# Optimization experiments

Hardware: AMD Instinct MI355X
Metric: run time of the kernel (lower is better)

Reference implementation:

```python
import jax, jax.numpy as jnp
import numpy as np
from jax import lax

B, J, I = 32, 48, 48          # batch, target len, source len
W = 2                          # target_window_size
CTX = 2 * W + 1                # 5
E, H = 128, 256                # embedding_size, hidden_units
VT, VS = 32000, 32000          # target / source vocab
S = 2 * J                      # HMM states (word + null)


def setup_inputs() -> dict:
    key = jax.random.key(0)
    ks = jax.random.split(key, 12)
    inp = {
        "target_embedding": jax.random.normal(ks[0], (VT, E), jnp.float32) * 0.02,
        "W_bridge": jax.random.normal(ks[1], (E * CTX, E), jnp.float32) * 0.02,
        "W_hidden": jax.random.normal(ks[2], (E, H), jnp.float32) * 0.02,
        "b_hidden": jnp.zeros((H,), jnp.float32),
        "W_vocab": jax.random.normal(ks[3], (H, VS), jnp.float32) * 0.02,
        "b_vocab": jnp.zeros((VS,), jnp.float32),
        "transition": jax.random.uniform(ks[4], (B, S, S), jnp.float32, 0.01, 1.0),
        "initial_transition": jax.random.uniform(ks[5], (B, S), jnp.float32, 0.01, 1.0),
        "targets_ctx": jax.random.randint(ks[6], (B, J * CTX), 0, VT, jnp.int32),
        "targets_ctx_null": jax.random.randint(ks[7], (B, J * CTX), 0, VT, jnp.int32),
        "sources": jax.random.randint(ks[8], (B, I), 0, VS, jnp.int32),
    }
    return inp


def _emission(emb, Wb, Wh, bh, Wv, bv, ctx_ids, sources):
    # embedding lookup + context reshape: [B, J*CTX, E] -> [B, J, CTX*E]
    x = emb[ctx_ids].reshape(ctx_ids.shape[0], -1, CTX * E)
    h = jnp.tanh(jnp.einsum('bjc,ce,eh->bjh', x, Wb, Wh) + bh)  # bridge+hidden
    probs = jax.nn.softmax(h @ Wv + bv, axis=-1)                # [B, J, VS]
    # per-example gather of source token columns -> [B, J, I]
    return jax.vmap(lambda p, s: p[:, s])(probs, sources)


def _forward_backward(pi, A, em):
    # pi [B,S], A [B,S,S], em [B,S,I]; scaled HMM forward-backward
    e = jnp.moveaxis(em, 2, 0)  # [I, B, S]
    a0 = pi * e[0]
    c0 = a0.sum(-1, keepdims=True)
    a0 = a0 / c0

    def fstep(a, ei):
        an = jnp.einsum('bs,bst->bt', a, A) * ei
        c = an.sum(-1, keepdims=True)
        an = an / c
        return an, (an, c)

    _, (alphas, cs) = lax.scan(fstep, a0, e[1:])
    alphas = jnp.concatenate([a0[None], alphas], 0)          # [I,B,S]
    cs = jnp.concatenate([c0[None], cs], 0)                  # [I,B,1]

    def bstep(b, inp):
        ei, ci = inp
        bn = jnp.einsum('bst,bt->bs', A, ei * b) / ci
        return bn, bn

    bI = jnp.ones_like(a0)
    _, betas_rev = lax.scan(bstep, bI, (e[1:][::-1], cs[1:][::-1]))
    betas = jnp.concatenate([betas_rev[::-1], bI[None]], 0)  # [I,B,S]

    gamma = alphas * betas                                   # state posteriors
    loglik = jnp.log(cs[..., 0]).sum(0)                      # [B]
    return jnp.moveaxis(gamma, 0, 2), loglik


def reference(target_embedding, W_bridge, W_hidden, b_hidden, W_vocab, b_vocab,
              transition, initial_transition, targets_ctx, targets_ctx_null, sources):
    em_word = _emission(target_embedding, W_bridge, W_hidden, b_hidden,
                        W_vocab, b_vocab, targets_ctx, sources)       # [B,J,I]
    em_null = _emission(target_embedding, W_bridge, W_hidden, b_hidden,
                        W_vocab, b_vocab, targets_ctx_null, sources)  # [B,J,I]
    emission = jnp.concatenate([em_word, em_null], axis=1)            # [B,2J,I]
    gamma, loglik = _forward_backward(initial_transition, transition, emission)
    return gamma, -loglik
```

## Files before the change

### kernel.cpp

```cpp
#include <hip/hip_runtime.h>
#include <hip/hip_bf16.h>

#define NB 32
#define NJ 48
#define NI 48
#define NCTX 5
#define NE 128
#define NH 256
#define NVS 32000
#define NS 96
#define NR 3072

typedef __attribute__((ext_vector_type(8))) short bf16x8;
typedef __attribute__((ext_vector_type(4))) float f32x4;

__device__ __forceinline__ unsigned short f2b(float f) {
  __hip_bfloat16 h = __float2bfloat16(f);
  return *reinterpret_cast<unsigned short*>(&h);
}
__device__ __forceinline__ float wave_sum(float v) {
  v += __shfl_xor(v, 1);
  v += __shfl_xor(v, 2);
  v += __shfl_xor(v, 4);
  v += __shfl_xor(v, 8);
  v += __shfl_xor(v, 16);
  v += __shfl_xor(v, 32);
  return v;
}
__device__ __forceinline__ void gload_lds16(const void* g, void* l) {
  __builtin_amdgcn_global_load_lds(
      (const __attribute__((address_space(1))) void*)g,
      (__attribute__((address_space(3))) void*)l, 16, 0, 0);
}


__global__ __launch_bounds__(256) void k_transpose(const float* __restrict__ Wv,
                                                   unsigned char* __restrict__ Wv8) {
  __shared__ float tile[64][65];
  int t = threadIdx.x;
  int v0 = blockIdx.x * 64, k0 = blockIdx.y * 64;
  {
    int kr = t >> 4, vq = t & 15;
#pragma unroll
    for (int it = 0; it < 4; ++it) {
      float4 v = *(const float4*)&Wv[(k0 + kr + 16 * it) * NVS + v0 + vq * 4];
      tile[kr + 16 * it][vq * 4 + 0] = v.x;
      tile[kr + 16 * it][vq * 4 + 1] = v.y;
      tile[kr + 16 * it][vq * 4 + 2] = v.z;
      tile[kr + 16 * it][vq * 4 + 3] = v.w;
    }
  }
  __syncthreads();
  {
    int vl = t >> 2, kq = t & 3;
    unsigned int q8[4];
#pragma unroll
    for (int d = 0; d < 4; ++d) {
      float f0 = tile[kq * 16 + d * 4 + 0][vl] * 64.0f;
      float f1 = tile[kq * 16 + d * 4 + 1][vl] * 64.0f;
      float f2 = tile[kq * 16 + d * 4 + 2][vl] * 64.0f;
      float f3 = tile[kq * 16 + d * 4 + 3][vl] * 64.0f;
      int w = __builtin_amdgcn_cvt_pk_fp8_f32(f0, f1, 0, false);
      w = __builtin_amdgcn_cvt_pk_fp8_f32(f2, f3, w, true);
      q8[d] = (unsigned int)w;
    }
    int kqp = kq ^ ((vl >> 2) & 3);
    unsigned int q8s[4];
    if ((vl >> 1) & 1) {
      q8s[0] = q8[2]; q8s[1] = q8[3]; q8s[2] = q8[0]; q8s[3] = q8[1];
    } else {
      q8s[0] = q8[0]; q8s[1] = q8[1]; q8s[2] = q8[2]; q8s[3] = q8[3];
    }
    *(uint4*)&Wv8[(v0 + vl) * 256 + k0 + kqp * 16] = *(uint4*)q8s;
  }
}

__global__ __launch_bounds__(256) void k_t2b(const float* __restrict__ src,
                                             unsigned short* __restrict__ dst,
                                             int R, int C) {
  __shared__ float tile[64][65];
  int t = threadIdx.x;
  int r0 = blockIdx.x * 64, c0 = blockIdx.y * 64;
  {
    int rr = t >> 4, cq = t & 15;
#pragma unroll
    for (int it = 0; it < 4; ++it) {
      float4 v = *(const float4*)&src[(r0 + rr + 16 * it) * C + c0 + cq * 4];
      tile[rr + 16 * it][cq * 4 + 0] = v.x;
      tile[rr + 16 * it][cq * 4 + 1] = v.y;
      tile[rr + 16 * it][cq * 4 + 2] = v.z;
      tile[rr + 16 * it][cq * 4 + 3] = v.w;
    }
  }
  __syncthreads();
  {
    int cc = t >> 2, rq = t & 3;
    unsigned short pk[16];
#pragma unroll
    for (int q = 0; q < 16; ++q) pk[q] = f2b(tile[rq * 16 + q][cc]);
    *(uint4*)&dst[(c0 + cc) * R + r0 + rq * 16] = *(uint4*)&pk[0];
    *(uint4*)&dst[(c0 + cc) * R + r0 + rq * 16 + 8] = *(uint4*)&pk[8];
  }
}

__global__ __launch_bounds__(256) void k_xb(const float* __restrict__ emb,
                                            const unsigned short* __restrict__ Wbt,
                                            const int* __restrict__ tc, const int* __restrict__ tcn,
                                            unsigned short* __restrict__ xb) {
  __shared__ unsigned short Ax[32 * 72];
  __shared__ unsigned short Bw[128 * 72];
  __shared__ unsigned short xout[32 * 136];
  int t = threadIdx.x;
  int r0 = blockIdx.x * 32;
  int wave = t >> 6, lane = t & 63;
  int wm = wave >> 1, wn = wave & 1;
  int lg = lane >> 4, lr = lane & 15;
  int arow = t >> 3, aseg = t & 7;
  int r = r0 + arow;
  int half = r / 1536, rem = r % 1536, bb = rem / 48, jj = rem % 48;
  const int* ids = half ? tcn : tc;
  int brow = t >> 1, bseg = t & 1;

  f32x4 acc[4];
#pragma unroll
  for (int n = 0; n < 4; ++n) acc[n] = (f32x4){0.f, 0.f, 0.f, 0.f};

  for (int step = 0; step < 10; ++step) {
    int k0 = step * 64;
    int p = step >> 1;
    int e0 = (step & 1) * 64;
    {
      int id = ids[bb * 240 + jj * 5 + p];
      const float4* er = (const float4*)&emb[id * 128 + e0 + aseg * 8];
      float4 v0 = er[0], v1 = er[1];
      unsigned short pk[8];
      pk[0] = f2b(v0.x); pk[1] = f2b(v0.y); pk[2] = f2b(v0.z); pk[3] = f2b(v0.w);
      pk[4] = f2b(v1.x); pk[5] = f2b(v1.y); pk[6] = f2b(v1.z); pk[7] = f2b(v1.w);
      *(uint4*)&Ax[arow * 72 + aseg * 8] = *(uint4*)&pk[0];
    }
    {
      const uint4* wp = (const uint4*)&Wbt[brow * 640 + k0 + bseg * 32];
      uint4* dp = (uint4*)&Bw[brow * 72 + bseg * 32];
      uint4 w0 = wp[0], w1 = wp[1], w2 = wp[2], w3 = wp[3];
      dp[0] = w0; dp[1] = w1; dp[2] = w2; dp[3] = w3;
    }
    __syncthreads();
#pragma unroll
    for (int kk = 0; kk < 2; ++kk) {
      bf16x8 a = *(const bf16x8*)&Ax[(wm * 16 + lr) * 72 + kk * 32 + lg * 8];
#pragma unroll
      for (int n = 0; n < 4; ++n) {
        bf16x8 b = *(const bf16x8*)&Bw[(wn * 64 + n * 16 + lr) * 72 + kk * 32 + lg * 8];
        acc[n] = __builtin_amdgcn_mfma_f32_16x16x32_bf16(a, b, acc[n], 0, 0, 0);
      }
    }
    __syncthreads();
  }
#pragma unroll
  for (int n = 0; n < 4; ++n)
#pragma unroll
    for (int g = 0; g < 4; ++g)
      xout[(wm * 16 + lg * 4 + g) * 136 + wn * 64 + n * 16 + lr] = f2b(acc[n][g]);
  __syncthreads();
  {
    int orow = t >> 3, os = t & 7;
    *(uint4*)&xb[(r0 + orow) * 128 + os * 16] = *(uint4*)&xout[orow * 136 + os * 16];
    *(uint4*)&xb[(r0 + orow) * 128 + os * 16 + 8] = *(uint4*)&xout[orow * 136 + os * 16 + 8];
  }
}

__global__ __launch_bounds__(256) void k_h(const unsigned short* __restrict__ xb,
                                           const unsigned short* __restrict__ Wht,
                                           const float* __restrict__ bh,
                                           unsigned char* __restrict__ hb8) {
  __shared__ char smem[69632];
  unsigned short* Asm = (unsigned short*)smem;
  unsigned short* Bsm = (unsigned short*)(smem + 34816);
  unsigned char* o8 = (unsigned char*)smem;
  int t = threadIdx.x;
  int r0 = blockIdx.x * 128, n0 = blockIdx.y * 128;
  int wave = t >> 6, lane = t & 63;
  int wm = wave >> 1, wn = wave & 1;
  int lg = lane >> 4, lr = lane & 15;
  {
    int row = t >> 1, seg = t & 1;
#pragma unroll
    for (int i = 0; i < 8; ++i) {
      *(uint4*)&Asm[row * 136 + seg * 64 + i * 8] = *(const uint4*)&xb[(r0 + row) * 128 + seg * 64 + i * 8];
      *(uint4*)&Bsm[row * 136 + seg * 64 + i * 8] = *(const uint4*)&Wht[(n0 + row) * 128 + seg * 64 + i * 8];
    }
  }
  __syncthreads();
  f32x4 acc[4][4];
#pragma unroll
  for (int m = 0; m < 4; ++m)
#pragma unroll
    for (int n = 0; n < 4; ++n) acc[m][n] = (f32x4){0.f, 0.f, 0.f, 0.f};
#pragma unroll
  for (int kk = 0; kk < 4; ++kk) {
    bf16x8 a[4], b[4];
#pragma unroll
    for (int m = 0; m < 4; ++m)
      a[m] = *(const bf16x8*)&Asm[(wm * 64 + m * 16 + lr) * 136 + kk * 32 + lg * 8];
#pragma unroll
    for (int n = 0; n < 4; ++n)
      b[n] = *(const bf16x8*)&Bsm[(wn * 64 + n * 16 + lr) * 136 + kk * 32 + lg * 8];
#pragma unroll
    for (int m = 0; m < 4; ++m)
#pragma unroll
      for (int n = 0; n < 4; ++n)
        acc[m][n] = __builtin_amdgcn_mfma_f32_16x16x32_bf16(a[m], b[n], acc[m][n], 0, 0, 0);
  }
  __syncthreads();
#pragma unroll
  for (int n = 0; n < 4; ++n) {
    int cl = wn * 64 + n * 16 + lr;
    float bvv = bh[n0 + cl];
#pragma unroll
    for (int m = 0; m < 4; ++m) {
#pragma unroll
      for (int g = 0; g < 4; ++g) {
        int rl = wm * 64 + m * 16 + lg * 4 + g;
        float hv = tanhf(acc[m][n][g] + bvv);
        int p8 = __builtin_amdgcn_cvt_pk_fp8_f32(hv * 256.0f, 0.0f, 0, false);
        o8[rl * 144 + cl] = (unsigned char)(p8 & 0xFF);
      }
    }
  }
  __syncthreads();
  {
    int row = t >> 1, seg = t & 1;
    int sig = (row >> 1) & 7;
    int swp = row & 1;
#pragma unroll
    for (int i = 0; i < 4; ++i) {
      int p_loc = seg * 4 + i;
      int w_loc = p_loc ^ sig;
      unsigned long long q[2];
      q[0] = *(const unsigned long long*)&o8[row * 144 + w_loc * 16 + swp * 8];
      q[1] = *(const unsigned long long*)&o8[row * 144 + w_loc * 16 + (swp ^ 1) * 8];
      *(uint4*)&hb8[(r0 + row) * 256 + n0 + p_loc * 16] = *(uint4*)q;
    }
  }
}

__global__ __launch_bounds__(256) void k_denom(const unsigned char* __restrict__ hb8,
                                               const unsigned char* __restrict__ Wv8,
                                               const float* __restrict__ bv,
                                               float* __restrict__ dpart) {
  __shared__ __align__(16) unsigned char Asm[32768];
  int t = threadIdx.x;
  int bid = blockIdx.x;
  int xcd = bid & 7;
  int pos = bid >> 3;
  int tile = xcd * 375 + pos;
  int vtp = tile / 24, rt = tile % 24;
  int r0 = rt * 128;
  int wave = t >> 6, lane = t & 63;
  int wm = wave >> 1, wn = wave & 1;
  int lg = lane >> 4, lr = lane & 15;

#pragma unroll
  for (int c = 0; c < 8; ++c) {
    int inst = wave * 8 + c;
    gload_lds16(&hb8[(r0 + inst * 4 + (lane >> 4)) * 256 + (lane & 15) * 16], &Asm[inst * 1024]);
  }
  __syncthreads();

  long long a_reg[4][8];
#pragma unroll
  for (int m = 0; m < 4; ++m) {
    int rowb = (wm * 64 + m * 16 + lr) * 256;
#pragma unroll
    for (int s = 0; s < 8; ++s)
      a_reg[m][s] = *(const long long*)&Asm[rowb + (((s * 4 + lg) ^ lr) << 3)];
  }

  const float SC = 6.103515625e-05f;
  int sg = (lr >> 1) & 7;

#pragma unroll
  for (int vt = 0; vt < 2; ++vt) {
    const unsigned char* Bp = Wv8 + ((size_t)((vtp * 2 + vt) * 128 + wn * 64 + lr)) * 256;
    f32x4 acc[4][4];
#pragma unroll
    for (int m = 0; m < 4; ++m)
#pragma unroll
      for (int n = 0; n < 4; ++n) acc[m][n] = (f32x4){0.f, 0.f, 0.f, 0.f};

#pragma unroll
    for (int ks = 0; ks < 4; ++ks) {
#pragma unroll
      for (int kk = 0; kk < 2; ++kk) {
        int so = ks * 64 + ((((kk << 2) + lg) ^ sg) << 3);
        long long b[4];
#pragma unroll
        for (int n = 0; n < 4; ++n)
          b[n] = *(const long long*)(Bp + n * 4096 + so);
        __builtin_amdgcn_s_setprio(1);
#pragma unroll
        for (int m = 0; m < 4; ++m)
#pragma unroll
          for (int n = 0; n < 4; ++n)
            acc[m][n] = __builtin_amdgcn_mfma_f32_16x16x32_fp8_fp8(a_reg[m][ks * 2 + kk], b[n],
                                                                   acc[m][n], 0, 0, 0);
        __builtin_amdgcn_s_setprio(0);
      }
    }
    int v0 = (vtp * 2 + vt) * 128;
    float rs[4][4];
#pragma unroll
    for (int m = 0; m < 4; ++m)
#pragma unroll
      for (int g = 0; g < 4; ++g) rs[m][g] = 0.f;
#pragma unroll
    for (int m = 0; m < 4; ++m) {
#pragma unroll
      for (int n = 0; n < 4; ++n) {
        float bvv = bv[v0 + wn * 64 + n * 16 + lr];
#pragma unroll
        for (int g = 0; g < 4; ++g) rs[m][g] += __expf(acc[m][n][g] * SC + bvv);
      }
    }
#pragma unroll
    for (int m = 0; m < 4; ++m)
#pragma unroll
      for (int g = 0; g < 4; ++g) {
        float v = rs[m][g];
        v += __shfl_xor(v, 1);
        v += __shfl_xor(v, 2);
        v += __shfl_xor(v, 4);
        v += __shfl_xor(v, 8);
        rs[m][g] = v;
      }
    if (lr == 0) {
      int d = (vtp * 2 + vt) * 2 + wn;
#pragma unroll
      for (int m = 0; m < 4; ++m)
#pragma unroll
        for (int g = 0; g < 4; ++g)
          dpart[d * NR + r0 + wm * 64 + m * 16 + lg * 4 + g] = rs[m][g];
    }
  }
}

__global__ void k_reduce(const float* __restrict__ dpart, float* __restrict__ dsum) {
  int r = blockIdx.x * 256 + threadIdx.x;
  float s = 0.f;
  for (int vt = 0; vt < 500; ++vt) s += dpart[vt * NR + r];
  dsum[r] = s;
}

__global__ __launch_bounds__(64) void k_emis(const unsigned char* __restrict__ hb8,
                                             const unsigned char* __restrict__ Wv8,
                                             const float* __restrict__ bv,
                                             const float* __restrict__ dsum,
                                             const int* __restrict__ src,
                                             float* __restrict__ em) {
  __shared__ unsigned char A8[48 * 256];
  __shared__ unsigned char B8[48 * 256];
  __shared__ int s_src[48];
  int t = threadIdx.x;
  int bh = blockIdx.x;
  int b = bh & 31, half = bh >> 5;
  int row4 = t >> 4, seg = t & 15;
  int rbase = half * 1536 + b * 48;
  if (t < 48) s_src[t] = src[b * 48 + t];
#pragma unroll
  for (int c = 0; c < 12; ++c) {
    int row = c * 4 + row4;
    gload_lds16(&hb8[(rbase + row) * 256 + seg * 16], &A8[c * 1024]);
    int sv = src[b * 48 + row];
    gload_lds16(&Wv8[sv * 256 + seg * 16], &B8[c * 1024]);
  }
  __syncthreads();
  int lg = t >> 4, lr = t & 15;
  int svr[3];
#pragma unroll
  for (int m = 0; m < 3; ++m) svr[m] = s_src[m * 16 + lr];
  f32x4 acc[3][3];
#pragma unroll
  for (int m = 0; m < 3; ++m)
#pragma unroll
    for (int n = 0; n < 3; ++n) acc[m][n] = (f32x4){0.f, 0.f, 0.f, 0.f};
#pragma unroll
  for (int kk = 0; kk < 8; ++kk) {
    int sa = kk * 4 + lg;
    long long a[3], bb[3];
#pragma unroll
    for (int m = 0; m < 3; ++m) {
      int rr = m * 16 + lr;
      a[m] = *(const long long*)&A8[rr * 256 + ((sa ^ lr) << 3)];
      bb[m] = *(const long long*)&B8[rr * 256 + ((sa >> 3) << 6) +
                                     (((sa & 7) ^ ((svr[m] >> 1) & 7)) << 3)];
    }
#pragma unroll
    for (int m = 0; m < 3; ++m)
#pragma unroll
      for (int n = 0; n < 3; ++n)
        acc[m][n] = __builtin_amdgcn_mfma_f32_16x16x32_fp8_fp8(a[m], bb[n], acc[m][n], 0, 0, 0);
  }
  const float SC = 6.103515625e-05f;
#pragma unroll
  for (int n = 0; n < 3; ++n) {
    int i = n * 16 + lr;
    float bvv = bv[svr[n]];
#pragma unroll
    for (int m = 0; m < 3; ++m) {
#pragma unroll
      for (int g = 0; g < 4; ++g) {
        int j = m * 16 + lg * 4 + g;
        float val = __expf(acc[m][n][g] * SC + bvv) / dsum[rbase + j];
        em[b * 4608 + (half * 48 + j) * 48 + i] = val;
      }
    }
  }
}

__global__ __launch_bounds__(192) void k_fb(const float* __restrict__ Atr, const float* __restrict__ pi,
                                            const float* __restrict__ em, float* __restrict__ alph,
                                            float* __restrict__ betas, float* __restrict__ out1) {
  __shared__ float A_st[96 * 97];
  __shared__ float em_lds[48 * 97];
  __shared__ __align__(16) float vec_lds[96];
  __shared__ float red[3];
  int t = threadIdx.x;
  int bid = blockIdx.x;
  int b = bid & 31;
  int role = bid >> 5;
  int col = t >> 1, half = t & 1;
  int base = b * 4608;

  for (int idx = t; idx < 96 * 96; idx += 192) {
    int s = idx / 96, tt = idx % 96;
    A_st[s * 97 + tt] = Atr[b * 9216 + idx];
  }
  for (int idx = t; idx < 96 * 48; idx += 192) {
    int s = idx / 48, i = idx % 48;
    em_lds[i * 97 + s] = em[base + idx];
  }
  __syncthreads();

  float Areg[48];
  if (role == 0) {
#pragma unroll
    for (int ss = 0; ss < 48; ++ss) Areg[ss] = A_st[(half * 48 + ss) * 97 + col];

    float llsum;
    {
      float v = pi[b * 96 + col] * em_lds[0 * 97 + col];
      float ws = half ? 0.f : v;
      ws = wave_sum(ws);
      if ((t & 63) == 0) red[t >> 6] = ws;
      __syncthreads();
      float c = red[0] + red[1] + red[2];
      float a = v / c;
      if (!half) {
        vec_lds[col] = a;
        alph[base + col] = a;
      }
      llsum = logf(c);
      __syncthreads();
    }
    for (int i = 1; i < 48; ++i) {
      float p = 0.f;
      const float4* ap = (const float4*)&vec_lds[half * 48];
#pragma unroll
      for (int q = 0; q < 12; ++q) {
        float4 av = ap[q];
        p += av.x * Areg[4 * q] + av.y * Areg[4 * q + 1] + av.z * Areg[4 * q + 2] + av.w * Areg[4 * q + 3];
      }
      p += __shfl_xor(p, 1);
      float an = p * em_lds[i * 97 + col];
      float ws = half ? 0.f : an;
      ws = wave_sum(ws);
      if ((t & 63) == 0) red[t >> 6] = ws;
      __syncthreads();
      float c = red[0] + red[1] + red[2];
      float a = an / c;
      if (!half) {
        vec_lds[col] = a;
        alph[base + i * 96 + col] = a;
      }
      llsum += logf(c);
      __syncthreads();
    }
    if (t == 0) out1[b] = -llsum;
  } else {
#pragma unroll
    for (int tt = 0; tt < 48; ++tt) Areg[tt] = A_st[col * 97 + half * 48 + tt];

    if (!half) {
      betas[base + 47 * 96 + col] = 1.0f;
      vec_lds[col] = em_lds[47 * 97 + col];
    }
    __syncthreads();
    for (int i = 46; i >= 0; --i) {
      float p = 0.f;
      const float4* ep = (const float4*)&vec_lds[half * 48];
#pragma unroll
      for (int q = 0; q < 12; ++q) {
        float4 ev = ep[q];
        p += ev.x * Areg[4 * q] + ev.y * Areg[4 * q + 1] + ev.z * Areg[4 * q + 2] + ev.w * Areg[4 * q + 3];
      }
      p += __shfl_xor(p, 1);
      float ws = half ? 0.f : p;
      ws = wave_sum(ws);
      if ((t & 63) == 0) red[t >> 6] = ws;
      __syncthreads();
      float c = red[0] + red[1] + red[2];
      float bt = p / c;
      if (!half) {
        betas[base + i * 96 + col] = bt;
        vec_lds[col] = em_lds[i * 97 + col] * bt;
      }
      __syncthreads();
    }
  }
}

__global__ __launch_bounds__(128) void k_gamma(const float* __restrict__ alph,
                                               const float* __restrict__ betas,
                                               float* __restrict__ out0) {
  __shared__ float red[2];
  int b = blockIdx.x, i = blockIdx.y;
  int t = threadIdx.x;
  float g = 0.f;
  if (t < 96) g = alph[b * 4608 + i * 96 + t] * betas[b * 4608 + i * 96 + t];
  float ws = wave_sum(g);
  if ((t & 63) == 0) red[t >> 6] = ws;
  __syncthreads();
  float c = red[0] + red[1];
  if (t < 96) out0[b * 4608 + t * 48 + i] = g / c;
}

extern "C" void kernel_launch(void* const* d_in, const int* in_sizes, int n_in,
                              void* d_out, int out_size, void* d_ws, size_t ws_size,
                              hipStream_t stream) {
  const float* emb = (const float*)d_in[0];
  const float* Wb  = (const float*)d_in[1];
  const float* Wh  = (const float*)d_in[2];
  const float* bh  = (const float*)d_in[3];
  const float* Wv  = (const float*)d_in[4];
  const float* bv  = (const float*)d_in[5];
  const float* Atr = (const float*)d_in[6];
  const float* pi  = (const float*)d_in[7];
  const int* tc    = (const int*)d_in[8];
  const int* tcn   = (const int*)d_in[9];
  const int* src   = (const int*)d_in[10];

  float* out0 = (float*)d_out;
  float* out1 = out0 + NB * NS * NI;

  char* ws = (char*)d_ws;
  unsigned char* wv8 = (unsigned char*)(ws);
  unsigned char* hb8 = (unsigned char*)(ws + 8192000);
  float* dpart       = (float*)(ws + 8978432);
  float* betas       = (float*)(ws + 8978432);
  float* dsum        = (float*)(ws + 15122432);
  float* em          = (float*)(ws + 15134720);
  float* alph        = (float*)(ws + 15724544);
  unsigned short* wbt = (unsigned short*)(ws + 16314368);
  unsigned short* wht = (unsigned short*)(ws + 16478208);
  unsigned short* xb  = (unsigned short*)(ws + 16543744);

  k_transpose<<<dim3(500, 4), 256, 0, stream>>>(Wv, wv8);
  k_t2b<<<dim3(10, 2), 256, 0, stream>>>(Wb, wbt, 640, 128);
  k_t2b<<<dim3(2, 4), 256, 0, stream>>>(Wh, wht, 128, 256);
  k_xb<<<96, 256, 0, stream>>>(emb, wbt, tc, tcn, xb);
  k_h<<<dim3(24, 2), 256, 0, stream>>>(xb, wht, bh, hb8);
  k_denom<<<3000, 256, 0, stream>>>(hb8, wv8, bv, dpart);
  k_reduce<<<12, 256, 0, stream>>>(dpart, dsum);
  k_emis<<<64, 64, 0, stream>>>(hb8, wv8, bv, dsum, src, em);
  k_fb<<<64, 192, 0, stream>>>(Atr, pi, em, alph, betas, out1);
  k_gamma<<<dim3(32, 48), 128, 0, stream>>>(alph, betas, out0);
}
```

Measured before the change: 168.8 us.

## Merge weight prep kernels, stage Wv8 through double-buffered LDS in denom, widen reduce

```diff
diff --git a/kernel.cpp b/kernel.cpp
--- a/kernel.cpp
+++ b/kernel.cpp
@@ -34,53 +34,11 @@
 }
 
 
-__global__ __launch_bounds__(256) void k_transpose(const float* __restrict__ Wv,
-                                                   unsigned char* __restrict__ Wv8) {
-  __shared__ float tile[64][65];
-  int t = threadIdx.x;
-  int v0 = blockIdx.x * 64, k0 = blockIdx.y * 64;
-  {
-    int kr = t >> 4, vq = t & 15;
-#pragma unroll
-    for (int it = 0; it < 4; ++it) {
-      float4 v = *(const float4*)&Wv[(k0 + kr + 16 * it) * NVS + v0 + vq * 4];
-      tile[kr + 16 * it][vq * 4 + 0] = v.x;
-      tile[kr + 16 * it][vq * 4 + 1] = v.y;
-      tile[kr + 16 * it][vq * 4 + 2] = v.z;
-      tile[kr + 16 * it][vq * 4 + 3] = v.w;
-    }
-  }
-  __syncthreads();
-  {
-    int vl = t >> 2, kq = t & 3;
-    unsigned int q8[4];
-#pragma unroll
-    for (int d = 0; d < 4; ++d) {
-      float f0 = tile[kq * 16 + d * 4 + 0][vl] * 64.0f;
-      float f1 = tile[kq * 16 + d * 4 + 1][vl] * 64.0f;
-      float f2 = tile[kq * 16 + d * 4 + 2][vl] * 64.0f;
-      float f3 = tile[kq * 16 + d * 4 + 3][vl] * 64.0f;
-      int w = __builtin_amdgcn_cvt_pk_fp8_f32(f0, f1, 0, false);
-      w = __builtin_amdgcn_cvt_pk_fp8_f32(f2, f3, w, true);
-      q8[d] = (unsigned int)w;
-    }
-    int kqp = kq ^ ((vl >> 2) & 3);
-    unsigned int q8s[4];
-    if ((vl >> 1) & 1) {
-      q8s[0] = q8[2]; q8s[1] = q8[3]; q8s[2] = q8[0]; q8s[3] = q8[1];
-    } else {
-      q8s[0] = q8[0]; q8s[1] = q8[1]; q8s[2] = q8[2]; q8s[3] = q8[3];
-    }
-    *(uint4*)&Wv8[(v0 + vl) * 256 + k0 + kqp * 16] = *(uint4*)q8s;
-  }
-}
-
-__global__ __launch_bounds__(256) void k_t2b(const float* __restrict__ src,
-                                             unsigned short* __restrict__ dst,
-                                             int R, int C) {
-  __shared__ float tile[64][65];
-  int t = threadIdx.x;
-  int r0 = blockIdx.x * 64, c0 = blockIdx.y * 64;
+__device__ __forceinline__ void t2b_body(const float* __restrict__ src,
+                                         unsigned short* __restrict__ dst,
+                                         int R, int C, int bx, int by, int t,
+                                         float (*tile)[65]) {
+  int r0 = bx * 64, c0 = by * 64;
   {
     int rr = t >> 4, cq = t & 15;
 #pragma unroll
@@ -100,6 +58,60 @@
     for (int q = 0; q < 16; ++q) pk[q] = f2b(tile[rq * 16 + q][cc]);
     *(uint4*)&dst[(c0 + cc) * R + r0 + rq * 16] = *(uint4*)&pk[0];
     *(uint4*)&dst[(c0 + cc) * R + r0 + rq * 16 + 8] = *(uint4*)&pk[8];
+  }
+}
+
+__global__ __launch_bounds__(256) void k_prep(const float* __restrict__ Wv,
+                                              unsigned char* __restrict__ Wv8,
+                                              const float* __restrict__ Wb,
+                                              unsigned short* __restrict__ wbt,
+                                              const float* __restrict__ Wh,
+                                              unsigned short* __restrict__ wht) {
+  __shared__ float tile[64][65];
+  int t = threadIdx.x;
+  int blk = blockIdx.x;
+  if (blk < 2000) {
+    int v0 = (blk % 500) * 64, k0 = (blk / 500) * 64;
+    {
+      int kr = t >> 4, vq = t & 15;
+#pragma unroll
+      for (int it = 0; it < 4; ++it) {
+        float4 v = *(const float4*)&Wv[(k0 + kr + 16 * it) * NVS + v0 + vq * 4];
+        tile[kr + 16 * it][vq * 4 + 0] = v.x;
+        tile[kr + 16 * it][vq * 4 + 1] = v.y;
+        tile[kr + 16 * it][vq * 4 + 2] = v.z;
+        tile[kr + 16 * it][vq * 4 + 3] = v.w;
+      }
+    }
+    __syncthreads();
+    {
+      int vl = t >> 2, kq = t & 3;
+      unsigned int q8[4];
+#pragma unroll
+      for (int d = 0; d < 4; ++d) {
+        float f0 = tile[kq * 16 + d * 4 + 0][vl] * 64.0f;
+        float f1 = tile[kq * 16 + d * 4 + 1][vl] * 64.0f;
+        float f2 = tile[kq * 16 + d * 4 + 2][vl] * 64.0f;
+        float f3 = tile[kq * 16 + d * 4 + 3][vl] * 64.0f;
+        int w = __builtin_amdgcn_cvt_pk_fp8_f32(f0, f1, 0, false);
+        w = __builtin_amdgcn_cvt_pk_fp8_f32(f2, f3, w, true);
+        q8[d] = (unsigned int)w;
+      }
+      int kqp = kq ^ ((vl >> 2) & 3);
+      unsigned int q8s[4];
+      if ((vl >> 1) & 1) {
+        q8s[0] = q8[2]; q8s[1] = q8[3]; q8s[2] = q8[0]; q8s[3] = q8[1];
+      } else {
+        q8s[0] = q8[0]; q8s[1] = q8[1]; q8s[2] = q8[2]; q8s[3] = q8[3];
+      }
+      *(uint4*)&Wv8[(v0 + vl) * 256 + k0 + kqp * 16] = *(uint4*)q8s;
+    }
+  } else if (blk < 2020) {
+    int b = blk - 2000;
+    t2b_body(Wb, wbt, 640, 128, b % 10, b / 10, t, tile);
+  } else {
+    int b = blk - 2020;
+    t2b_body(Wh, wht, 128, 256, b % 2, b / 2, t, tile);
   }
 }
 
@@ -248,107 +260,137 @@
                                                const unsigned char* __restrict__ Wv8,
                                                const float* __restrict__ bv,
                                                float* __restrict__ dpart) {
-  __shared__ __align__(16) unsigned char Asm[32768];
+  __shared__ __align__(16) unsigned char smem[16384];
   int t = threadIdx.x;
   int bid = blockIdx.x;
   int xcd = bid & 7;
   int pos = bid >> 3;
-  int tile = xcd * 375 + pos;
-  int vtp = tile / 24, rt = tile % 24;
+  int tl = xcd * 375 + pos;
+  int vtp = tl / 24, rt = tl % 24;
   int r0 = rt * 128;
   int wave = t >> 6, lane = t & 63;
   int wm = wave >> 1, wn = wave & 1;
   int lg = lane >> 4, lr = lane & 15;
 
 #pragma unroll
-  for (int c = 0; c < 8; ++c) {
-    int inst = wave * 8 + c;
-    gload_lds16(&hb8[(r0 + inst * 4 + (lane >> 4)) * 256 + (lane & 15) * 16], &Asm[inst * 1024]);
-  }
-  __syncthreads();
+  for (int c = 0; c < 2; ++c) {
+    int i = wave * 2 + c;
+    gload_lds16(&Wv8[((size_t)(vtp * 256 + i * 16 + (lane >> 2))) * 256 + (lane & 3) * 16],
+                smem + i * 1024);
+  }
 
   long long a_reg[4][8];
 #pragma unroll
   for (int m = 0; m < 4; ++m) {
-    int rowb = (wm * 64 + m * 16 + lr) * 256;
-#pragma unroll
-    for (int s = 0; s < 8; ++s)
-      a_reg[m][s] = *(const long long*)&Asm[rowb + (((s * 4 + lg) ^ lr) << 3)];
+#pragma unroll
+    for (int c = 0; c < 2; ++c) {
+      int inst = wave * 2 + c;
+      int slot = inst * 4 + (lane >> 4);
+      int row = (slot & 15) + m * 16 + ((slot >> 4) << 6);
+      gload_lds16(&hb8[(size_t)(r0 + row) * 256 + (lane & 15) * 16],
+                  smem + 8192 + inst * 1024);
+    }
+    __syncthreads();
+    {
+      int q = lr + 16 * wm;
+#pragma unroll
+      for (int s = 0; s < 8; ++s)
+        a_reg[m][s] = *(const long long*)&smem[8192 + q * 256 + (((s * 4 + lg) ^ lr) << 3)];
+    }
+    __syncthreads();
   }
 
   const float SC = 6.103515625e-05f;
-  int sg = (lr >> 1) & 7;
-
-#pragma unroll
-  for (int vt = 0; vt < 2; ++vt) {
-    const unsigned char* Bp = Wv8 + ((size_t)((vtp * 2 + vt) * 128 + wn * 64 + lr)) * 256;
-    f32x4 acc[4][4];
-#pragma unroll
-    for (int m = 0; m < 4; ++m)
-#pragma unroll
-      for (int n = 0; n < 4; ++n) acc[m][n] = (f32x4){0.f, 0.f, 0.f, 0.f};
-
-#pragma unroll
-    for (int ks = 0; ks < 4; ++ks) {
-#pragma unroll
-      for (int kk = 0; kk < 2; ++kk) {
-        int so = ks * 64 + ((((kk << 2) + lg) ^ sg) << 3);
-        long long b[4];
+  f32x4 acc[4][4];
+#pragma unroll
+  for (int m = 0; m < 4; ++m)
+#pragma unroll
+    for (int n = 0; n < 4; ++n) acc[m][n] = (f32x4){0.f, 0.f, 0.f, 0.f};
+
+#pragma unroll
+  for (int s = 0; s < 8; ++s) {
+    if (s < 7) {
+      int ns = s + 1;
+      int nvt = ns >> 2, nks = ns & 3;
+#pragma unroll
+      for (int c = 0; c < 2; ++c) {
+        int i = wave * 2 + c;
+        gload_lds16(&Wv8[((size_t)((vtp * 2 + nvt) * 128 + i * 16 + (lane >> 2))) * 256 +
+                         nks * 64 + (lane & 3) * 16],
+                    smem + ((ns & 1) << 13) + i * 1024);
+      }
+    }
+    int ks = s & 3;
+    const unsigned char* bp = smem + ((s & 1) << 13);
+#pragma unroll
+    for (int kk = 0; kk < 2; ++kk) {
+      long long b[4];
+#pragma unroll
+      for (int n = 0; n < 4; ++n) {
+        int rr = wn * 64 + n * 16 + lr;
+        b[n] = *(const long long*)&bp[rr * 64 + ((((kk << 2) + lg) ^ ((lr >> 1) & 7)) << 3)];
+      }
+      __builtin_amdgcn_s_setprio(1);
+#pragma unroll
+      for (int m = 0; m < 4; ++m)
 #pragma unroll
         for (int n = 0; n < 4; ++n)
-          b[n] = *(const long long*)(Bp + n * 4096 + so);
-        __builtin_amdgcn_s_setprio(1);
+          acc[m][n] = __builtin_amdgcn_mfma_f32_16x16x32_fp8_fp8(a_reg[m][ks * 2 + kk], b[n],
+                                                                 acc[m][n], 0, 0, 0);
+      __builtin_amdgcn_s_setprio(0);
+    }
+    if (ks == 3) {
+      int vt = s >> 2;
+      int v0 = (vtp * 2 + vt) * 128;
+      float rs[4][4];
+#pragma unroll
+      for (int m = 0; m < 4; ++m)
+#pragma unroll
+        for (int g = 0; g < 4; ++g) rs[m][g] = 0.f;
+#pragma unroll
+      for (int m = 0; m < 4; ++m) {
+#pragma unroll
+        for (int n = 0; n < 4; ++n) {
+          float bvv = bv[v0 + wn * 64 + n * 16 + lr];
+#pragma unroll
+          for (int g = 0; g < 4; ++g) rs[m][g] += __expf(acc[m][n][g] * SC + bvv);
+          acc[m][n] = (f32x4){0.f, 0.f, 0.f, 0.f};
+        }
+      }
+#pragma unroll
+      for (int m = 0; m < 4; ++m)
+#pragma unroll
+        for (int g = 0; g < 4; ++g) {
+          float v = rs[m][g];
+          v += __shfl_xor(v, 1);
+          v += __shfl_xor(v, 2);
+          v += __shfl_xor(v, 4);
+          v += __shfl_xor(v, 8);
+          rs[m][g] = v;
+        }
+      if (lr == 0) {
+        int d = (vtp * 2 + vt) * 2 + wn;
 #pragma unroll
         for (int m = 0; m < 4; ++m)
 #pragma unroll
-          for (int n = 0; n < 4; ++n)
-            acc[m][n] = __builtin_amdgcn_mfma_f32_16x16x32_fp8_fp8(a_reg[m][ks * 2 + kk], b[n],
-                                                                   acc[m][n], 0, 0, 0);
-        __builtin_amdgcn_s_setprio(0);
-      }
-    }
-    int v0 = (vtp * 2 + vt) * 128;
-    float rs[4][4];
-#pragma unroll
-    for (int m = 0; m < 4; ++m)
-#pragma unroll
-      for (int g = 0; g < 4; ++g) rs[m][g] = 0.f;
-#pragma unroll
-    for (int m = 0; m < 4; ++m) {
-#pragma unroll
-      for (int n = 0; n < 4; ++n) {
-        float bvv = bv[v0 + wn * 64 + n * 16 + lr];
-#pragma unroll
-        for (int g = 0; g < 4; ++g) rs[m][g] += __expf(acc[m][n][g] * SC + bvv);
-      }
-    }
-#pragma unroll
-    for (int m = 0; m < 4; ++m)
-#pragma unroll
-      for (int g = 0; g < 4; ++g) {
-        float v = rs[m][g];
-        v += __shfl_xor(v, 1);
-        v += __shfl_xor(v, 2);
-        v += __shfl_xor(v, 4);
-        v += __shfl_xor(v, 8);
-        rs[m][g] = v;
-      }
-    if (lr == 0) {
-      int d = (vtp * 2 + vt) * 2 + wn;
-#pragma unroll
-      for (int m = 0; m < 4; ++m)
-#pragma unroll
-        for (int g = 0; g < 4; ++g)
-          dpart[d * NR + r0 + wm * 64 + m * 16 + lg * 4 + g] = rs[m][g];
-    }
-  }
-}
-
-__global__ void k_reduce(const float* __restrict__ dpart, float* __restrict__ dsum) {
-  int r = blockIdx.x * 256 + threadIdx.x;
+          for (int g = 0; g < 4; ++g)
+            dpart[(size_t)d * NR + r0 + wm * 64 + m * 16 + lg * 4 + g] = rs[m][g];
+      }
+    }
+    __syncthreads();
+  }
+}
+
+__global__ __launch_bounds__(256) void k_reduce(const float* __restrict__ dpart,
+                                                float* __restrict__ dsum) {
+  int t = threadIdx.x;
+  int r = blockIdx.x * 64 + (t >> 2);
+  int q = t & 3;
   float s = 0.f;
-  for (int vt = 0; vt < 500; ++vt) s += dpart[vt * NR + r];
-  dsum[r] = s;
+  for (int vt = q; vt < 500; vt += 4) s += dpart[(size_t)vt * NR + r];
+  s += __shfl_xor(s, 1);
+  s += __shfl_xor(s, 2);
+  if (q == 0) dsum[r] = s;
 }
 
 __global__ __launch_bounds__(64) void k_emis(const unsigned char* __restrict__ hb8,
@@ -564,13 +606,11 @@
   unsigned short* wht = (unsigned short*)(ws + 16478208);
   unsigned short* xb  = (unsigned short*)(ws + 16543744);
 
-  k_transpose<<<dim3(500, 4), 256, 0, stream>>>(Wv, wv8);
-  k_t2b<<<dim3(10, 2), 256, 0, stream>>>(Wb, wbt, 640, 128);
-  k_t2b<<<dim3(2, 4), 256, 0, stream>>>(Wh, wht, 128, 256);
+  k_prep<<<2028, 256, 0, stream>>>(Wv, wv8, Wb, wbt, Wh, wht);
   k_xb<<<96, 256, 0, stream>>>(emb, wbt, tc, tcn, xb);
   k_h<<<dim3(24, 2), 256, 0, stream>>>(xb, wht, bh, hb8);
   k_denom<<<3000, 256, 0, stream>>>(hb8, wv8, bv, dpart);
-  k_reduce<<<12, 256, 0, stream>>>(dpart, dsum);
+  k_reduce<<<48, 256, 0, stream>>>(dpart, dsum);
   k_emis<<<64, 64, 0, stream>>>(hb8, wv8, bv, dsum, src, em);
   k_fb<<<64, 192, 0, stream>>>(Atr, pi, em, alph, betas, out1);
   k_gamma<<<dim3(32, 48), 128, 0, stream>>>(alph, betas, out0);
```

Result: slower. 174.2 us (+3.2%).
